# Performance work log

Measured on AMD Instinct MI355X. Metric: run time of the kernel, lower is better.

Reference implementation:

```python
import jax, jax.numpy as jnp
import numpy as np

B, NQ, NV = 4, 16384, 16384
DIM, FRAMES = 64, 4
D = DIM * FRAMES            # embed_dims = 256
HEADS, POINTS, LEVELS = 8, 4, 1
HD = D // HEADS             # head_dim = 32
HL, WL = 128, 128           # single-level feature map, HL*WL == NV
EPS = 1e-6


def setup_inputs() -> dict:
    key = jax.random.key(0)
    ks = jax.random.split(key, 14)
    inp = {
        "query": jax.random.normal(ks[0], (B, NQ, D), jnp.float32),
        "feat": jax.random.normal(ks[1], (B, NV, D), jnp.float32),
        "reference_points": jax.random.uniform(ks[2], (B, NQ, LEVELS, 2), jnp.float32),
        "spatial_shapes": jnp.array([[HL, WL]], jnp.int32),
        "level_start_index": jnp.array([0], jnp.int32),
        # LayerNorm params
        "qn_scale": jnp.ones((D,), jnp.float32),
        "qn_bias": jnp.zeros((D,), jnp.float32),
        "fn_scale": jnp.ones((D,), jnp.float32),
        "fn_bias": jnp.zeros((D,), jnp.float32),
        # MSDeformAttn projections
        "W_value": jax.random.normal(ks[3], (D, D), jnp.float32) / np.sqrt(D),
        "b_value": jnp.zeros((D,), jnp.float32),
        "W_off": jax.random.normal(ks[4], (D, HEADS * LEVELS * POINTS * 2), jnp.float32) * 0.01,
        "b_off": jax.random.normal(ks[5], (HEADS * LEVELS * POINTS * 2,), jnp.float32) * 0.5,
        "W_attn": jax.random.normal(ks[6], (D, HEADS * LEVELS * POINTS), jnp.float32) * 0.02,
        "b_attn": jnp.zeros((HEADS * LEVELS * POINTS,), jnp.float32),
        "W_out": jax.random.normal(ks[7], (D, D), jnp.float32) / np.sqrt(D),
        "b_out": jnp.zeros((D,), jnp.float32),
        # gamma is a learned scale (init 0 in the module; randomized here so it contributes)
        "gamma": jax.random.normal(ks[8], (D,), jnp.float32) * 0.1,
    }
    return inp


def _layer_norm(x, scale, bias):
    mu = jnp.mean(x, axis=-1, keepdims=True)
    var = jnp.mean(jnp.square(x - mu), axis=-1, keepdims=True)
    return (x - mu) * jax.lax.rsqrt(var + EPS) * scale + bias


def _bilinear_gather(v, loc, Hl, Wl):
    # v:   [B, H, N, hd] flattened level values (row-major HxW)
    # loc: [B, H, NQ, P, 2] normalized sampling locations in [0,1]
    # grid_sample semantics: align_corners=False, zero padding
    x = loc[..., 0] * Wl - 0.5
    y = loc[..., 1] * Hl - 0.5
    x0 = jnp.floor(x); y0 = jnp.floor(y)
    x1 = x0 + 1.0;     y1 = y0 + 1.0
    wx1 = x - x0; wx0 = 1.0 - wx1
    wy1 = y - y0; wy0 = 1.0 - wy1
    out = 0.0
    for xi, yi, w in ((x0, y0, wx0 * wy0), (x1, y0, wx1 * wy0),
                      (x0, y1, wx0 * wy1), (x1, y1, wx1 * wy1)):
        inb = (xi >= 0) & (xi < Wl) & (yi >= 0) & (yi < Hl)
        idx = (jnp.clip(yi, 0, Hl - 1) * Wl + jnp.clip(xi, 0, Wl - 1)).astype(jnp.int32)
        Bc, Hc, NQc, Pc = idx.shape
        g = jnp.take_along_axis(v, idx.reshape(Bc, Hc, NQc * Pc)[..., None], axis=2)
        g = g.reshape(Bc, Hc, NQc, Pc, -1)          # [B, H, NQ, P, hd]
        out = out + g * (w * inb)[..., None]
    return out


def reference(query, feat, reference_points, spatial_shapes, level_start_index,
              qn_scale, qn_bias, fn_scale, fn_bias,
              W_value, b_value, W_off, b_off, W_attn, b_attn, W_out, b_out, gamma):
    Bq, nq, _ = query.shape
    q = _layer_norm(query, qn_scale, qn_bias)
    v = _layer_norm(feat, fn_scale, fn_bias)

    # value projection -> per-head values [B, H, NV, hd]
    value = (v @ W_value + b_value).reshape(Bq, -1, HEADS, HD).transpose(0, 2, 1, 3)

    # sampling offsets [B, NQ, H, L, P, 2] and attention weights (softmax over L*P)
    off = (q @ W_off + b_off).reshape(Bq, nq, HEADS, LEVELS, POINTS, 2)
    aw = jax.nn.softmax((q @ W_attn + b_attn).reshape(Bq, nq, HEADS, LEVELS * POINTS), axis=-1)
    aw = aw.reshape(Bq, nq, HEADS, LEVELS, POINTS)

    ss = np.asarray(spatial_shapes)          # static level geometry
    lsi = np.asarray(level_start_index)
    offset_norm = ss[:, ::-1].astype(np.float32)  # (W, H) per level
    # sampling locations [B, NQ, H, L, P, 2]
    loc = reference_points[:, :, None, :, None, :] + off / offset_norm[None, None, None, :, None, :]

    acc = jnp.zeros((Bq, HEADS, nq, HD), query.dtype)
    for l in range(LEVELS):
        Hl, Wl = int(ss[l, 0]), int(ss[l, 1])
        start = int(lsi[l])
        v_l = value[:, :, start:start + Hl * Wl]                # [B, H, Hl*Wl, hd]
        loc_l = loc[:, :, :, l].transpose(0, 2, 1, 3, 4)        # [B, H, NQ, P, 2]
        sampled = _bilinear_gather(v_l, loc_l, Hl, Wl)          # [B, H, NQ, P, hd]
        aw_l = aw[:, :, :, l].transpose(0, 2, 1, 3)             # [B, H, NQ, P]
        acc = acc + jnp.einsum('bhnpd,bhnp->bhnd', sampled, aw_l)

    out = acc.transpose(0, 2, 1, 3).reshape(Bq, nq, D) @ W_out + b_out
    return query + gamma * out
```

## Files before the change

### kernel.cpp

```cpp
#include <hip/hip_runtime.h>

#define NQ 16384
#define NV 16384
#define DMODEL 256

typedef __bf16 bf16x8 __attribute__((ext_vector_type(8)));
typedef float f32x4 __attribute__((ext_vector_type(4)));

__device__ __forceinline__ unsigned short f2bf(float x) {
    union { float f; unsigned int u; } v; v.f = x;
    unsigned int r = v.u + 0x7fff + ((v.u >> 16) & 1);
    return (unsigned short)(r >> 16);
}
__device__ __forceinline__ float blo(unsigned int u) {
    union { unsigned int u; float f; } v; v.u = u << 16; return v.f;
}
__device__ __forceinline__ float bhi(unsigned int u) {
    union { unsigned int u; float f; } v; v.u = u & 0xFFFF0000u; return v.f;
}
__device__ __forceinline__ f32x4 mfma16(bf16x8 a, bf16x8 b, f32x4 c) {
    return __builtin_amdgcn_mfma_f32_16x16x32_bf16(a, b, c, 0, 0, 0);
}

__device__ __forceinline__ void ln_stage_half(
    const float* __restrict__ src, const float4* sc, const float4* bi,
    unsigned short* A, int g_row0, int l_row0, int g, int li) {
    float4 x[4][4];
#pragma unroll
    for (int it = 0; it < 4; ++it) {
        const size_t row = (size_t)(g_row0 + it * 4 + g);
#pragma unroll
        for (int j = 0; j < 4; ++j)
            x[it][j] = *(const float4*)(src + row * 256 + li * 16 + j * 4);
    }
#pragma unroll
    for (int it = 0; it < 4; ++it) {
        float s = 0.f, sq = 0.f;
#pragma unroll
        for (int j = 0; j < 4; ++j) {
            s  += x[it][j].x + x[it][j].y + x[it][j].z + x[it][j].w;
            sq += x[it][j].x * x[it][j].x + x[it][j].y * x[it][j].y +
                  x[it][j].z * x[it][j].z + x[it][j].w * x[it][j].w;
        }
#pragma unroll
        for (int d = 1; d < 16; d <<= 1) {
            s  += __shfl_xor(s, d);
            sq += __shfl_xor(sq, d);
        }
        float mu = s * 0.00390625f;
        float rstd = rsqrtf(sq * 0.00390625f - mu * mu + 1e-6f);
        unsigned int pk[8];
#pragma unroll
        for (int j = 0; j < 4; ++j) {
            pk[2 * j] = (unsigned)f2bf((x[it][j].x - mu) * rstd * sc[j].x + bi[j].x) |
                        ((unsigned)f2bf((x[it][j].y - mu) * rstd * sc[j].y + bi[j].y) << 16);
            pk[2 * j + 1] = (unsigned)f2bf((x[it][j].z - mu) * rstd * sc[j].z + bi[j].z) |
                            ((unsigned)f2bf((x[it][j].w - mu) * rstd * sc[j].w + bi[j].w) << 16);
        }
        uint4* dst = (uint4*)&A[(l_row0 + it * 4 + g) * 264 + li * 16];
        dst[0] = make_uint4(pk[0], pk[1], pk[2], pk[3]);
        dst[1] = make_uint4(pk[4], pk[5], pk[6], pk[7]);
    }
}

__global__ __launch_bounds__(256) void k_prep(
    const float* __restrict__ Wv, const float* __restrict__ Woff,
    const float* __restrict__ Wattn, const float* __restrict__ Wout,
    unsigned short* __restrict__ WtV, unsigned short* __restrict__ WtC,
    unsigned short* __restrict__ WtO) {
    int t = blockIdx.x * 256 + threadIdx.x;
    if (t < 256 * 256) { int n = t >> 8, k = t & 255; WtV[t] = f2bf(Wv[k * 256 + n]); return; }
    t -= 256 * 256;
    if (t < 256 * 256) { int n = t >> 8, k = t & 255; WtO[t] = f2bf(Wout[k * 256 + n]); return; }
    t -= 256 * 256;
    if (t < 96 * 256) {
        int j = t >> 8, k = t & 255;
        float w = (j < 64) ? Woff[k * 64 + j] : Wattn[k * 32 + (j - 64)];
        WtC[j * 256 + k] = f2bf(w);
    }
}

__global__ __launch_bounds__(256) void k_ln_value(
    const float* __restrict__ feat, const float* __restrict__ fn_scale,
    const float* __restrict__ fn_bias, const float* __restrict__ b_value,
    const unsigned short* __restrict__ WtV, unsigned short* __restrict__ value) {
    __shared__ unsigned short A[128 * 264];
    const int lane = threadIdx.x & 63;
    const int w = threadIdx.x >> 6;
    const int m0 = blockIdx.x * 128;
    const int g = lane >> 4, li = lane & 15;
    {
        float4 sc[4], bi[4];
#pragma unroll
        for (int j = 0; j < 4; ++j) {
            sc[j] = *(const float4*)(fn_scale + li * 16 + j * 4);
            bi[j] = *(const float4*)(fn_bias + li * 16 + j * 4);
        }
        ln_stage_half(feat, sc, bi, A, m0 + w * 32, w * 32, g, li);
        ln_stage_half(feat, sc, bi, A, m0 + w * 32 + 16, w * 32 + 16, g, li);
    }
    __syncthreads();
    const int lrow = lane & 15, lk = (lane >> 4) * 8;
    f32x4 acc[4][8];
#pragma unroll
    for (int i = 0; i < 4; ++i)
#pragma unroll
        for (int m = 0; m < 8; ++m) acc[i][m] = (f32x4){0.f, 0.f, 0.f, 0.f};

#define LOADB_V(dst, kk)                                                              \
    _Pragma("unroll") for (int i = 0; i < 4; ++i) dst[i] =                            \
        *(const bf16x8*)(WtV + (size_t)((w * 4 + i) * 16 + lrow) * 256 + (kk) * 32 + lk);
#define MFMA_STEP_V(bf, kk)                                                           \
    _Pragma("unroll") for (int m = 0; m < 8; ++m) {                                   \
        bf16x8 a = *(const bf16x8*)&A[(m * 16 + lrow) * 264 + (kk) * 32 + lk];        \
        _Pragma("unroll") for (int i = 0; i < 4; ++i)                                 \
            acc[i][m] = mfma16(bf[i], a, acc[i][m]);                                  \
    }
    {
        bf16x8 b0[4], b1[4];
        LOADB_V(b0, 0)
#pragma unroll
        for (int k2 = 0; k2 < 4; ++k2) {
            LOADB_V(b1, k2 * 2 + 1)
            MFMA_STEP_V(b0, k2 * 2)
            if (k2 < 3) { LOADB_V(b0, k2 * 2 + 2) }
            MFMA_STEP_V(b1, k2 * 2 + 1)
        }
    }
#pragma unroll
    for (int i = 0; i < 4; ++i) {
        const int col0 = (w * 4 + i) * 16 + (lane >> 4) * 4;
        float4 bv = *(const float4*)(b_value + col0);
#pragma unroll
        for (int m = 0; m < 8; ++m) {
            const size_t row = (size_t)(m0 + m * 16 + (lane & 15));
            uint2 r;
            r.x = (unsigned)f2bf(acc[i][m][0] + bv.x) | ((unsigned)f2bf(acc[i][m][1] + bv.y) << 16);
            r.y = (unsigned)f2bf(acc[i][m][2] + bv.z) | ((unsigned)f2bf(acc[i][m][3] + bv.w) << 16);
            *(uint2*)(value + row * 256 + col0) = r;
        }
    }
}

__global__ __launch_bounds__(256) void k_ln_qoff(
    const float* __restrict__ query, const float* __restrict__ qn_scale,
    const float* __restrict__ qn_bias, const float* __restrict__ refpt,
    const float* __restrict__ b_off, const float* __restrict__ b_attn,
    const unsigned short* __restrict__ WtC, float4* __restrict__ samples) {
    __shared__ unsigned short A[128 * 264];
    const int lane = threadIdx.x & 63;
    const int w = threadIdx.x >> 6;
    const int m0 = blockIdx.x * 128;
    const int g = lane >> 4, li = lane & 15;
    {
        float4 sc[4], bi[4];
#pragma unroll
        for (int j = 0; j < 4; ++j) {
            sc[j] = *(const float4*)(qn_scale + li * 16 + j * 4);
            bi[j] = *(const float4*)(qn_bias + li * 16 + j * 4);
        }
        ln_stage_half(query, sc, bi, A, m0 + w * 32, w * 32, g, li);
        ln_stage_half(query, sc, bi, A, m0 + w * 32 + 16, w * 32 + 16, g, li);
    }
    __syncthreads();
    const int lrow = lane & 15, lk = (lane >> 4) * 8;
    f32x4 acc[6][2];
#pragma unroll
    for (int i = 0; i < 6; ++i)
#pragma unroll
        for (int m = 0; m < 2; ++m) acc[i][m] = (f32x4){0.f, 0.f, 0.f, 0.f};

#define LOADB_Q(dst, kk)                                                              \
    _Pragma("unroll") for (int i = 0; i < 6; ++i) dst[i] =                            \
        *(const bf16x8*)(WtC + (size_t)(i * 16 + lrow) * 256 + (kk) * 32 + lk);
#define MFMA_STEP_Q(bf, kk)                                                           \
    _Pragma("unroll") for (int m = 0; m < 2; ++m) {                                   \
        bf16x8 a = *(const bf16x8*)&A[(w * 32 + m * 16 + lrow) * 264 + (kk) * 32 + lk]; \
        _Pragma("unroll") for (int i = 0; i < 6; ++i)                                 \
            acc[i][m] = mfma16(bf[i], a, acc[i][m]);                                  \
    }
    {
        bf16x8 b0[6], b1[6];
        LOADB_Q(b0, 0)
#pragma unroll
        for (int k2 = 0; k2 < 4; ++k2) {
            LOADB_Q(b1, k2 * 2 + 1)
            MFMA_STEP_Q(b0, k2 * 2)
            if (k2 < 3) { LOADB_Q(b0, k2 * 2 + 2) }
            MFMA_STEP_Q(b1, k2 * 2 + 1)
        }
    }
    __syncthreads();
    float* Dl = (float*)A + w * 4224;
#pragma unroll
    for (int i = 0; i < 6; ++i) {
        const int col0 = i * 16 + (lane >> 4) * 4;
#pragma unroll
        for (int m = 0; m < 2; ++m) {
            const int rl = m * 16 + (lane & 15);
            *(float4*)&Dl[rl * 100 + col0] =
                make_float4(acc[i][m][0], acc[i][m][1], acc[i][m][2], acc[i][m][3]);
        }
    }
    __syncthreads();
#pragma unroll
    for (int it = 0; it < 4; ++it) {
        int idx = it * 64 + lane;
        int rl = idx >> 3;
        int h = idx & 7;
        int row = m0 + w * 32 + rl;
        float rx = refpt[(size_t)row * 2 + 0] * 128.f - 0.5f;
        float ry = refpt[(size_t)row * 2 + 1] * 128.f - 0.5f;
        float l0 = Dl[rl * 100 + 64 + h * 4 + 0] + b_attn[h * 4 + 0];
        float l1 = Dl[rl * 100 + 64 + h * 4 + 1] + b_attn[h * 4 + 1];
        float l2 = Dl[rl * 100 + 64 + h * 4 + 2] + b_attn[h * 4 + 2];
        float l3 = Dl[rl * 100 + 64 + h * 4 + 3] + b_attn[h * 4 + 3];
        float mx = fmaxf(fmaxf(l0, l1), fmaxf(l2, l3));
        float e0 = __expf(l0 - mx), e1 = __expf(l1 - mx);
        float e2 = __expf(l2 - mx), e3 = __expf(l3 - mx);
        float inv = 1.f / (e0 + e1 + e2 + e3);
        float ww[4] = {e0 * inv, e1 * inv, e2 * inv, e3 * inv};
#pragma unroll
        for (int p = 0; p < 4; ++p) {
            float ox = Dl[rl * 100 + h * 8 + p * 2 + 0] + b_off[h * 8 + p * 2 + 0];
            float oy = Dl[rl * 100 + h * 8 + p * 2 + 1] + b_off[h * 8 + p * 2 + 1];
            samples[((size_t)row * 8 + h) * 4 + p] = make_float4(rx + ox, ry + oy, ww[p], 0.f);
        }
    }
}

__global__ __launch_bounds__(256) void k_gather(
    const unsigned short* __restrict__ value, const float4* __restrict__ samples,
    unsigned short* __restrict__ accb) {
    const int tid = blockIdx.x * 256 + threadIdx.x;
    const int sub = tid & 3;
    const int t = tid >> 2;
    const int h = t & 7;
    const int bq = t >> 3;
    const int b = bq >> 14;
    const unsigned short* vb = value + ((size_t)b << 14) * 256 + h * 32 + sub * 8;
    float a0 = 0.f, a1 = 0.f, a2 = 0.f, a3 = 0.f;
    float a4 = 0.f, a5 = 0.f, a6 = 0.f, a7 = 0.f;
#pragma unroll
    for (int p = 0; p < 4; ++p) {
        float4 s = samples[(size_t)t * 4 + p];
        float xf = floorf(s.x), yf = floorf(s.y);
        float fx = s.x - xf, fy = s.y - yf;
        int x0 = (int)xf, y0 = (int)yf;
        int x1 = x0 + 1, y1 = y0 + 1;
        float wgt = s.z;
        bool bx0 = (unsigned)x0 < 128u, bx1 = (unsigned)x1 < 128u;
        bool by0 = (unsigned)y0 < 128u, by1 = (unsigned)y1 < 128u;
        float wt[4];
        wt[0] = (bx0 && by0) ? (1.f - fx) * (1.f - fy) * wgt : 0.f;
        wt[1] = (bx1 && by0) ? fx * (1.f - fy) * wgt : 0.f;
        wt[2] = (bx0 && by1) ? (1.f - fx) * fy * wgt : 0.f;
        wt[3] = (bx1 && by1) ? fx * fy * wgt : 0.f;
        int xc0 = min(max(x0, 0), 127), xc1 = min(max(x1, 0), 127);
        int yc0 = min(max(y0, 0), 127), yc1 = min(max(y1, 0), 127);
        int pix[4];
        pix[0] = yc0 * 128 + xc0; pix[1] = yc0 * 128 + xc1;
        pix[2] = yc1 * 128 + xc0; pix[3] = yc1 * 128 + xc1;
#pragma unroll
        for (int tp = 0; tp < 4; ++tp) {
            uint4 u = *(const uint4*)(vb + (size_t)pix[tp] * 256);
            float w = wt[tp];
            a0 = fmaf(w, blo(u.x), a0); a1 = fmaf(w, bhi(u.x), a1);
            a2 = fmaf(w, blo(u.y), a2); a3 = fmaf(w, bhi(u.y), a3);
            a4 = fmaf(w, blo(u.z), a4); a5 = fmaf(w, bhi(u.z), a5);
            a6 = fmaf(w, blo(u.w), a6); a7 = fmaf(w, bhi(u.w), a7);
        }
    }
    uint4 r;
    r.x = (unsigned)f2bf(a0) | ((unsigned)f2bf(a1) << 16);
    r.y = (unsigned)f2bf(a2) | ((unsigned)f2bf(a3) << 16);
    r.z = (unsigned)f2bf(a4) | ((unsigned)f2bf(a5) << 16);
    r.w = (unsigned)f2bf(a6) | ((unsigned)f2bf(a7) << 16);
    *(uint4*)(accb + (size_t)bq * 256 + h * 32 + sub * 8) = r;
}

__global__ __launch_bounds__(256) void k_out(
    const unsigned short* __restrict__ accb, const unsigned short* __restrict__ WtO,
    const float* __restrict__ b_out, const float* __restrict__ gamma,
    const float* __restrict__ query, float* __restrict__ out) {
    __shared__ unsigned short A[128 * 264];
    const int m0 = blockIdx.x * 128;
    {
        const int c = threadIdx.x & 31;
        const int r0 = threadIdx.x >> 5;
#pragma unroll
        for (int i = 0; i < 16; ++i) {
            const int r = r0 + i * 8;
            *(uint4*)&A[r * 264 + c * 8] = *(const uint4*)(accb + (size_t)(m0 + r) * 256 + c * 8);
        }
    }
    __syncthreads();
    const int lane = threadIdx.x & 63;
    const int w = threadIdx.x >> 6;
    const int lrow = lane & 15, lk = (lane >> 4) * 8;
    f32x4 acc[4][8];
#pragma unroll
    for (int i = 0; i < 4; ++i)
#pragma unroll
        for (int m = 0; m < 8; ++m) acc[i][m] = (f32x4){0.f, 0.f, 0.f, 0.f};

#define LOADB_O(dst, kk)                                                              \
    _Pragma("unroll") for (int i = 0; i < 4; ++i) dst[i] =                            \
        *(const bf16x8*)(WtO + (size_t)((w * 4 + i) * 16 + lrow) * 256 + (kk) * 32 + lk);
    {
        bf16x8 b0[4], b1[4];
        LOADB_O(b0, 0)
#pragma unroll
        for (int k2 = 0; k2 < 4; ++k2) {
            LOADB_O(b1, k2 * 2 + 1)
            MFMA_STEP_V(b0, k2 * 2)
            if (k2 < 3) { LOADB_O(b0, k2 * 2 + 2) }
            MFMA_STEP_V(b1, k2 * 2 + 1)
        }
    }
#pragma unroll
    for (int i = 0; i < 4; ++i) {
        const int col0 = (w * 4 + i) * 16 + (lane >> 4) * 4;
        float4 bo = *(const float4*)(b_out + col0);
        float4 gm = *(const float4*)(gamma + col0);
#pragma unroll
        for (int m = 0; m < 8; ++m) {
            const size_t row = (size_t)(m0 + m * 16 + (lane & 15));
            float4 q = *(const float4*)(query + row * 256 + col0);
            float4 o;
            o.x = q.x + gm.x * (acc[i][m][0] + bo.x);
            o.y = q.y + gm.y * (acc[i][m][1] + bo.y);
            o.z = q.z + gm.z * (acc[i][m][2] + bo.z);
            o.w = q.w + gm.w * (acc[i][m][3] + bo.w);
            *(float4*)(out + row * 256 + col0) = o;
        }
    }
}

extern "C" void kernel_launch(void* const* d_in, const int* in_sizes, int n_in,
                              void* d_out, int out_size, void* d_ws, size_t ws_size,
                              hipStream_t stream) {
    const float* query    = (const float*)d_in[0];
    const float* feat     = (const float*)d_in[1];
    const float* refpt    = (const float*)d_in[2];
    const float* qn_scale = (const float*)d_in[5];
    const float* qn_bias  = (const float*)d_in[6];
    const float* fn_scale = (const float*)d_in[7];
    const float* fn_bias  = (const float*)d_in[8];
    const float* W_value  = (const float*)d_in[9];
    const float* b_value  = (const float*)d_in[10];
    const float* W_off    = (const float*)d_in[11];
    const float* b_off    = (const float*)d_in[12];
    const float* W_attn   = (const float*)d_in[13];
    const float* b_attn   = (const float*)d_in[14];
    const float* W_out    = (const float*)d_in[15];
    const float* b_out    = (const float*)d_in[16];
    const float* gamma    = (const float*)d_in[17];
    float* out = (float*)d_out;

    char* ws = (char*)d_ws;
    unsigned short* WtV   = (unsigned short*)(ws);
    unsigned short* WtO   = (unsigned short*)(ws + 131072);
    unsigned short* WtC   = (unsigned short*)(ws + 262144);
    unsigned short* value = (unsigned short*)(ws + 311296);
    float4*        samples = (float4*)(ws + 311296 + 33554432);
    unsigned short* accb  = (unsigned short*)(ws + 311296 + 67108864);

    hipLaunchKernelGGL(k_prep, dim3(608), dim3(256), 0, stream,
                       W_value, W_off, W_attn, W_out, WtV, WtC, WtO);
    hipLaunchKernelGGL(k_ln_value, dim3(512), dim3(256), 0, stream,
                       feat, fn_scale, fn_bias, b_value, WtV, value);
    hipLaunchKernelGGL(k_ln_qoff, dim3(512), dim3(256), 0, stream,
                       query, qn_scale, qn_bias, refpt, b_off, b_attn, WtC, samples);
    hipLaunchKernelGGL(k_gather, dim3(8192), dim3(256), 0, stream,
                       value, samples, accb);
    hipLaunchKernelGGL(k_out, dim3(512), dim3(256), 0, stream,
                       accb, WtO, b_out, gamma, query, out);
}
```

Measured before the change: 177.8 us.

## Split LayerNorm into a standalone high-parallelism kernel feeding bf16 GEMM kernels

LayerNorm of feat and query moves out of the two projection kernels into one k_ln kernel with 4096 small blocks, which writes bf16 normalized rows to workspace. The value and offset/attention GEMM kernels then just copy those bf16 tiles into LDS. The aim is to hide the fp32 load latency that the large-LDS, 512-block GEMM kernels hid poorly while they normalized their own inputs. The cost is an extra round trip of the bf16 activations through global memory plus one more launch. The workspace is reorganised so the LN buffers alias samples and accb, and the epilogues hoist the bias and gamma loads and reorder their loops.

```diff
diff --git a/kernel.cpp b/kernel.cpp
--- a/kernel.cpp
+++ b/kernel.cpp
@@ -20,47 +20,6 @@
 }
 __device__ __forceinline__ f32x4 mfma16(bf16x8 a, bf16x8 b, f32x4 c) {
     return __builtin_amdgcn_mfma_f32_16x16x32_bf16(a, b, c, 0, 0, 0);
-}
-
-__device__ __forceinline__ void ln_stage_half(
-    const float* __restrict__ src, const float4* sc, const float4* bi,
-    unsigned short* A, int g_row0, int l_row0, int g, int li) {
-    float4 x[4][4];
-#pragma unroll
-    for (int it = 0; it < 4; ++it) {
-        const size_t row = (size_t)(g_row0 + it * 4 + g);
-#pragma unroll
-        for (int j = 0; j < 4; ++j)
-            x[it][j] = *(const float4*)(src + row * 256 + li * 16 + j * 4);
-    }
-#pragma unroll
-    for (int it = 0; it < 4; ++it) {
-        float s = 0.f, sq = 0.f;
-#pragma unroll
-        for (int j = 0; j < 4; ++j) {
-            s  += x[it][j].x + x[it][j].y + x[it][j].z + x[it][j].w;
-            sq += x[it][j].x * x[it][j].x + x[it][j].y * x[it][j].y +
-                  x[it][j].z * x[it][j].z + x[it][j].w * x[it][j].w;
-        }
-#pragma unroll
-        for (int d = 1; d < 16; d <<= 1) {
-            s  += __shfl_xor(s, d);
-            sq += __shfl_xor(sq, d);
-        }
-        float mu = s * 0.00390625f;
-        float rstd = rsqrtf(sq * 0.00390625f - mu * mu + 1e-6f);
-        unsigned int pk[8];
-#pragma unroll
-        for (int j = 0; j < 4; ++j) {
-            pk[2 * j] = (unsigned)f2bf((x[it][j].x - mu) * rstd * sc[j].x + bi[j].x) |
-                        ((unsigned)f2bf((x[it][j].y - mu) * rstd * sc[j].y + bi[j].y) << 16);
-            pk[2 * j + 1] = (unsigned)f2bf((x[it][j].z - mu) * rstd * sc[j].z + bi[j].z) |
-                            ((unsigned)f2bf((x[it][j].w - mu) * rstd * sc[j].w + bi[j].w) << 16);
-        }
-        uint4* dst = (uint4*)&A[(l_row0 + it * 4 + g) * 264 + li * 16];
-        dst[0] = make_uint4(pk[0], pk[1], pk[2], pk[3]);
-        dst[1] = make_uint4(pk[4], pk[5], pk[6], pk[7]);
-    }
 }
 
 __global__ __launch_bounds__(256) void k_prep(
@@ -80,42 +39,98 @@
     }
 }
 
-__global__ __launch_bounds__(256) void k_ln_value(
-    const float* __restrict__ feat, const float* __restrict__ fn_scale,
-    const float* __restrict__ fn_bias, const float* __restrict__ b_value,
-    const unsigned short* __restrict__ WtV, unsigned short* __restrict__ value) {
-    __shared__ unsigned short A[128 * 264];
+__global__ __launch_bounds__(256) void k_ln(
+    const float* __restrict__ feat, const float* __restrict__ query,
+    const float* __restrict__ fns, const float* __restrict__ fnb,
+    const float* __restrict__ qns, const float* __restrict__ qnb,
+    unsigned short* __restrict__ lnf, unsigned short* __restrict__ lnq) {
+    const int blk = blockIdx.x;
+    const float* src; const float* scale; const float* bias; unsigned short* dst;
+    int row0;
+    if (blk < 2048) { src = feat;  scale = fns; bias = fnb; dst = lnf; row0 = blk * 32; }
+    else            { src = query; scale = qns; bias = qnb; dst = lnq; row0 = (blk - 2048) * 32; }
     const int lane = threadIdx.x & 63;
     const int w = threadIdx.x >> 6;
-    const int m0 = blockIdx.x * 128;
     const int g = lane >> 4, li = lane & 15;
-    {
-        float4 sc[4], bi[4];
+    float4 sc[4], bi[4];
+#pragma unroll
+    for (int j = 0; j < 4; ++j) {
+        sc[j] = *(const float4*)(scale + li * 16 + j * 4);
+        bi[j] = *(const float4*)(bias + li * 16 + j * 4);
+    }
+    const int r0 = row0 + w * 8 + g;
+    float4 x[2][4];
+#pragma unroll
+    for (int h2 = 0; h2 < 2; ++h2)
+#pragma unroll
+        for (int j = 0; j < 4; ++j)
+            x[h2][j] = *(const float4*)(src + (size_t)(r0 + h2 * 4) * 256 + li * 16 + j * 4);
+#pragma unroll
+    for (int h2 = 0; h2 < 2; ++h2) {
+        float s = 0.f, sq = 0.f;
 #pragma unroll
         for (int j = 0; j < 4; ++j) {
-            sc[j] = *(const float4*)(fn_scale + li * 16 + j * 4);
-            bi[j] = *(const float4*)(fn_bias + li * 16 + j * 4);
-        }
-        ln_stage_half(feat, sc, bi, A, m0 + w * 32, w * 32, g, li);
-        ln_stage_half(feat, sc, bi, A, m0 + w * 32 + 16, w * 32 + 16, g, li);
-    }
-    __syncthreads();
-    const int lrow = lane & 15, lk = (lane >> 4) * 8;
-    f32x4 acc[4][8];
-#pragma unroll
-    for (int i = 0; i < 4; ++i)
-#pragma unroll
-        for (int m = 0; m < 8; ++m) acc[i][m] = (f32x4){0.f, 0.f, 0.f, 0.f};
-
-#define LOADB_V(dst, kk)                                                              \
-    _Pragma("unroll") for (int i = 0; i < 4; ++i) dst[i] =                            \
-        *(const bf16x8*)(WtV + (size_t)((w * 4 + i) * 16 + lrow) * 256 + (kk) * 32 + lk);
+            s  += x[h2][j].x + x[h2][j].y + x[h2][j].z + x[h2][j].w;
+            sq += x[h2][j].x * x[h2][j].x + x[h2][j].y * x[h2][j].y +
+                  x[h2][j].z * x[h2][j].z + x[h2][j].w * x[h2][j].w;
+        }
+#pragma unroll
+        for (int d = 1; d < 16; d <<= 1) {
+            s  += __shfl_xor(s, d);
+            sq += __shfl_xor(sq, d);
+        }
+        float mu = s * 0.00390625f;
+        float rstd = rsqrtf(sq * 0.00390625f - mu * mu + 1e-6f);
+        unsigned int pk[8];
+#pragma unroll
+        for (int j = 0; j < 4; ++j) {
+            pk[2 * j] = (unsigned)f2bf((x[h2][j].x - mu) * rstd * sc[j].x + bi[j].x) |
+                        ((unsigned)f2bf((x[h2][j].y - mu) * rstd * sc[j].y + bi[j].y) << 16);
+            pk[2 * j + 1] = (unsigned)f2bf((x[h2][j].z - mu) * rstd * sc[j].z + bi[j].z) |
+                            ((unsigned)f2bf((x[h2][j].w - mu) * rstd * sc[j].w + bi[j].w) << 16);
+        }
+        uint4* dstp = (uint4*)(dst + (size_t)(r0 + h2 * 4) * 256 + li * 16);
+        dstp[0] = make_uint4(pk[0], pk[1], pk[2], pk[3]);
+        dstp[1] = make_uint4(pk[4], pk[5], pk[6], pk[7]);
+    }
+}
+
+#define STAGE_A(srcbuf)                                                               \
+    {                                                                                 \
+        const int c = threadIdx.x & 31;                                               \
+        const int rt = threadIdx.x >> 5;                                              \
+        _Pragma("unroll") for (int i = 0; i < 16; ++i) {                              \
+            const int r = rt + i * 8;                                                 \
+            *(uint4*)&A[r * 264 + c * 8] =                                            \
+                *(const uint4*)((srcbuf) + (size_t)(m0 + r) * 256 + c * 8);           \
+        }                                                                             \
+    }
+
 #define MFMA_STEP_V(bf, kk)                                                           \
     _Pragma("unroll") for (int m = 0; m < 8; ++m) {                                   \
         bf16x8 a = *(const bf16x8*)&A[(m * 16 + lrow) * 264 + (kk) * 32 + lk];        \
         _Pragma("unroll") for (int i = 0; i < 4; ++i)                                 \
             acc[i][m] = mfma16(bf[i], a, acc[i][m]);                                  \
     }
+
+__global__ __launch_bounds__(256) void k_value(
+    const unsigned short* __restrict__ lnf, const float* __restrict__ b_value,
+    const unsigned short* __restrict__ WtV, unsigned short* __restrict__ value) {
+    __shared__ unsigned short A[128 * 264];
+    const int m0 = blockIdx.x * 128;
+    STAGE_A(lnf)
+    __syncthreads();
+    const int lane = threadIdx.x & 63;
+    const int w = threadIdx.x >> 6;
+    const int lrow = lane & 15, lk = (lane >> 4) * 8;
+    f32x4 acc[4][8];
+#pragma unroll
+    for (int i = 0; i < 4; ++i)
+#pragma unroll
+        for (int m = 0; m < 8; ++m) acc[i][m] = (f32x4){0.f, 0.f, 0.f, 0.f};
+#define LOADB_V(dst, kk)                                                              \
+    _Pragma("unroll") for (int i = 0; i < 4; ++i) dst[i] =                            \
+        *(const bf16x8*)(WtV + (size_t)((w * 4 + i) * 16 + lrow) * 256 + (kk) * 32 + lk);
     {
         bf16x8 b0[4], b1[4];
         LOADB_V(b0, 0)
@@ -127,49 +142,40 @@
             MFMA_STEP_V(b1, k2 * 2 + 1)
         }
     }
-#pragma unroll
-    for (int i = 0; i < 4; ++i) {
-        const int col0 = (w * 4 + i) * 16 + (lane >> 4) * 4;
-        float4 bv = *(const float4*)(b_value + col0);
-#pragma unroll
-        for (int m = 0; m < 8; ++m) {
-            const size_t row = (size_t)(m0 + m * 16 + (lane & 15));
+    const int g = lane >> 4;
+    float4 bv[4];
+#pragma unroll
+    for (int i = 0; i < 4; ++i) bv[i] = *(const float4*)(b_value + (w * 4 + i) * 16 + g * 4);
+#pragma unroll
+    for (int m = 0; m < 8; ++m) {
+        const size_t row = (size_t)(m0 + m * 16 + (lane & 15));
+#pragma unroll
+        for (int i = 0; i < 4; ++i) {
+            const int col0 = (w * 4 + i) * 16 + g * 4;
             uint2 r;
-            r.x = (unsigned)f2bf(acc[i][m][0] + bv.x) | ((unsigned)f2bf(acc[i][m][1] + bv.y) << 16);
-            r.y = (unsigned)f2bf(acc[i][m][2] + bv.z) | ((unsigned)f2bf(acc[i][m][3] + bv.w) << 16);
+            r.x = (unsigned)f2bf(acc[i][m][0] + bv[i].x) | ((unsigned)f2bf(acc[i][m][1] + bv[i].y) << 16);
+            r.y = (unsigned)f2bf(acc[i][m][2] + bv[i].z) | ((unsigned)f2bf(acc[i][m][3] + bv[i].w) << 16);
             *(uint2*)(value + row * 256 + col0) = r;
         }
     }
 }
 
-__global__ __launch_bounds__(256) void k_ln_qoff(
-    const float* __restrict__ query, const float* __restrict__ qn_scale,
-    const float* __restrict__ qn_bias, const float* __restrict__ refpt,
+__global__ __launch_bounds__(256) void k_qoff(
+    const unsigned short* __restrict__ lnq, const float* __restrict__ refpt,
     const float* __restrict__ b_off, const float* __restrict__ b_attn,
     const unsigned short* __restrict__ WtC, float4* __restrict__ samples) {
     __shared__ unsigned short A[128 * 264];
+    const int m0 = blockIdx.x * 128;
+    STAGE_A(lnq)
+    __syncthreads();
     const int lane = threadIdx.x & 63;
     const int w = threadIdx.x >> 6;
-    const int m0 = blockIdx.x * 128;
-    const int g = lane >> 4, li = lane & 15;
-    {
-        float4 sc[4], bi[4];
-#pragma unroll
-        for (int j = 0; j < 4; ++j) {
-            sc[j] = *(const float4*)(qn_scale + li * 16 + j * 4);
-            bi[j] = *(const float4*)(qn_bias + li * 16 + j * 4);
-        }
-        ln_stage_half(query, sc, bi, A, m0 + w * 32, w * 32, g, li);
-        ln_stage_half(query, sc, bi, A, m0 + w * 32 + 16, w * 32 + 16, g, li);
-    }
-    __syncthreads();
     const int lrow = lane & 15, lk = (lane >> 4) * 8;
     f32x4 acc[6][2];
 #pragma unroll
     for (int i = 0; i < 6; ++i)
 #pragma unroll
         for (int m = 0; m < 2; ++m) acc[i][m] = (f32x4){0.f, 0.f, 0.f, 0.f};
-
 #define LOADB_Q(dst, kk)                                                              \
     _Pragma("unroll") for (int i = 0; i < 6; ++i) dst[i] =                            \
         *(const bf16x8*)(WtC + (size_t)(i * 16 + lrow) * 256 + (kk) * 32 + lk);
@@ -285,15 +291,7 @@
     const float* __restrict__ query, float* __restrict__ out) {
     __shared__ unsigned short A[128 * 264];
     const int m0 = blockIdx.x * 128;
-    {
-        const int c = threadIdx.x & 31;
-        const int r0 = threadIdx.x >> 5;
-#pragma unroll
-        for (int i = 0; i < 16; ++i) {
-            const int r = r0 + i * 8;
-            *(uint4*)&A[r * 264 + c * 8] = *(const uint4*)(accb + (size_t)(m0 + r) * 256 + c * 8);
-        }
-    }
+    STAGE_A(accb)
     __syncthreads();
     const int lane = threadIdx.x & 63;
     const int w = threadIdx.x >> 6;
@@ -303,7 +301,6 @@
     for (int i = 0; i < 4; ++i)
 #pragma unroll
         for (int m = 0; m < 8; ++m) acc[i][m] = (f32x4){0.f, 0.f, 0.f, 0.f};
-
 #define LOADB_O(dst, kk)                                                              \
     _Pragma("unroll") for (int i = 0; i < 4; ++i) dst[i] =                            \
         *(const bf16x8*)(WtO + (size_t)((w * 4 + i) * 16 + lrow) * 256 + (kk) * 32 + lk);
@@ -318,20 +315,25 @@
             MFMA_STEP_V(b1, k2 * 2 + 1)
         }
     }
+    const int g = lane >> 4;
+    float4 bo[4], gm[4];
 #pragma unroll
     for (int i = 0; i < 4; ++i) {
-        const int col0 = (w * 4 + i) * 16 + (lane >> 4) * 4;
-        float4 bo = *(const float4*)(b_out + col0);
-        float4 gm = *(const float4*)(gamma + col0);
-#pragma unroll
-        for (int m = 0; m < 8; ++m) {
-            const size_t row = (size_t)(m0 + m * 16 + (lane & 15));
+        bo[i] = *(const float4*)(b_out + (w * 4 + i) * 16 + g * 4);
+        gm[i] = *(const float4*)(gamma + (w * 4 + i) * 16 + g * 4);
+    }
+#pragma unroll
+    for (int m = 0; m < 8; ++m) {
+        const size_t row = (size_t)(m0 + m * 16 + (lane & 15));
+#pragma unroll
+        for (int i = 0; i < 4; ++i) {
+            const int col0 = (w * 4 + i) * 16 + g * 4;
             float4 q = *(const float4*)(query + row * 256 + col0);
             float4 o;
-            o.x = q.x + gm.x * (acc[i][m][0] + bo.x);
-            o.y = q.y + gm.y * (acc[i][m][1] + bo.y);
-            o.z = q.z + gm.z * (acc[i][m][2] + bo.z);
-            o.w = q.w + gm.w * (acc[i][m][3] + bo.w);
+            o.x = q.x + gm[i].x * (acc[i][m][0] + bo[i].x);
+            o.y = q.y + gm[i].y * (acc[i][m][1] + bo[i].y);
+            o.z = q.z + gm[i].z * (acc[i][m][2] + bo[i].z);
+            o.w = q.w + gm[i].w * (acc[i][m][3] + bo[i].w);
             *(float4*)(out + row * 256 + col0) = o;
         }
     }
@@ -363,15 +365,21 @@
     unsigned short* WtO   = (unsigned short*)(ws + 131072);
     unsigned short* WtC   = (unsigned short*)(ws + 262144);
     unsigned short* value = (unsigned short*)(ws + 311296);
-    float4*        samples = (float4*)(ws + 311296 + 33554432);
-    unsigned short* accb  = (unsigned short*)(ws + 311296 + 67108864);
+    char* regA = ws + 311296 + 33554432;
+    char* regB = ws + 311296 + 2 * 33554432;
+    unsigned short* lnf     = (unsigned short*)regA;
+    float4*         samples = (float4*)regA;
+    unsigned short* lnq     = (unsigned short*)regB;
+    unsigned short* accb    = (unsigned short*)regB;
 
     hipLaunchKernelGGL(k_prep, dim3(608), dim3(256), 0, stream,
                        W_value, W_off, W_attn, W_out, WtV, WtC, WtO);
-    hipLaunchKernelGGL(k_ln_value, dim3(512), dim3(256), 0, stream,
-                       feat, fn_scale, fn_bias, b_value, WtV, value);
-    hipLaunchKernelGGL(k_ln_qoff, dim3(512), dim3(256), 0, stream,
-                       query, qn_scale, qn_bias, refpt, b_off, b_attn, WtC, samples);
+    hipLaunchKernelGGL(k_ln, dim3(4096), dim3(256), 0, stream,
+                       feat, query, fn_scale, fn_bias, qn_scale, qn_bias, lnf, lnq);
+    hipLaunchKernelGGL(k_value, dim3(512), dim3(256), 0, stream,
+                       lnf, b_value, WtV, value);
+    hipLaunchKernelGGL(k_qoff, dim3(512), dim3(256), 0, stream,
+                       lnq, refpt, b_off, b_attn, WtC, samples);
     hipLaunchKernelGGL(k_gather, dim3(8192), dim3(256), 0, stream,
                        value, samples, accb);
     hipLaunchKernelGGL(k_out, dim3(512), dim3(256), 0, stream,
```

New measurement: 190.9 us. 1.07x slower.
